# Performance work log

Measured on AMD Instinct MI355X. Metric: run time of the kernel, lower is better.

Reference implementation:

```python
import jax, jax.numpy as jnp
import numpy as np
import math

NUM_EMBED = 1024
EMBED_DIM = 256
COMMITMENT_COST = 0.25


def setup_inputs() -> dict:
    key = jax.random.key(0)
    k1, k2 = jax.random.split(key)
    inputs = jax.random.normal(k1, (16, EMBED_DIM, 4096), dtype=jnp.float32)
    embed = jax.random.normal(k2, (NUM_EMBED, EMBED_DIM), dtype=jnp.float32)
    return {"inputs": inputs, "embed": embed}


def reference(inputs, embed):
    sg = jax.lax.stop_gradient
    num_embed = embed.shape[0]
    # channels-first (B, D, T) -> (B, T, D)
    x = jnp.swapaxes(inputs, 1, -1)
    B, T, D = x.shape
    flat = x.reshape(-1, D)  # (N, D)
    # pairwise squared distances to the codebook: (N, K)
    d2 = (jnp.sum(flat * flat, axis=1, keepdims=True)
          + jnp.sum(embed * embed, axis=1)
          - 2.0 * flat @ embed.T)
    q_idx = jnp.argmin(d2, axis=1)  # (N,) int
    # one-hot @ embed is just a gather of the nearest codewords
    z_q = embed[q_idx].reshape(x.shape)  # (B, T, D)
    vq_loss = jnp.mean((z_q - sg(x)) ** 2)
    commitment_loss = jnp.mean((sg(z_q) - x) ** 2)
    loss = vq_loss + COMMITMENT_COST * commitment_loss
    # straight-through estimator
    z_q_st = x + sg(z_q - x)
    # codebook usage stats: probs = mean of the one-hot rows
    n = flat.shape[0]
    probs = jnp.zeros((num_embed,), dtype=flat.dtype).at[q_idx].add(1.0) / n
    perplexity = jnp.exp(-jnp.sum(probs * jnp.log(probs + 1e-10)))
    num_spatial_positions = n / B  # == T
    kldiv_r = (math.log(num_embed) * num_spatial_positions
               * jnp.ones((B, 1), dtype=x.dtype))
    z_q_out = jnp.swapaxes(z_q_st, 1, -1)  # back to (B, D, T)
    return z_q_out, loss, kldiv_r, perplexity
```

## Files before the change

### kernel.cpp

```cpp
#include <hip/hip_runtime.h>
#include <math.h>

#define T_DIM 4096
#define D_DIM 256
#define K_NUM 1024
#define B_NUM 16
#define N_TOT (B_NUM * T_DIM)
#define EPS_FLAG 0.25f

typedef float f32x4 __attribute__((ext_vector_type(4)));
typedef _Float16 half8 __attribute__((ext_vector_type(8)));

#define WS_FLAGCNT 0
#define WS_LOSS 4
#define WS_DONE 8
#define WS_HIST 64
#define WS_E2 4352
#define WS_QIDX 8704
#define WS_FLAGLIST 270848
#define WS_BESTD 532992
#define WS_ESWZ 795136
#define WS_XROWS 1319424

__device__ inline unsigned umin_(unsigned a, unsigned b) { return a < b ? a : b; }
__device__ inline unsigned umax_(unsigned a, unsigned b) { return a > b ? a : b; }

__global__ __launch_bounds__(256) void prep_kernel(const float* __restrict__ embed,
                                                   unsigned char* __restrict__ eswz,
                                                   float* __restrict__ e2,
                                                   int* __restrict__ wszero) {
    const int tid = threadIdx.x;
    if (blockIdx.x == 0) {
        #pragma unroll
        for (int i = tid; i < 1040; i += 256) wszero[i] = 0;
    }
    const int col = blockIdx.x * 8 + (tid >> 5);
    const int c = tid & 31;
    const float* src = embed + (size_t)col * D_DIM + c * 8;
    half8 h;
    float s = 0.f;
    #pragma unroll
    for (int j = 0; j < 8; ++j) {
        float v = src[j];
        h[j] = (_Float16)v;
        s = fmaf(v, v, s);
    }
    const int g = col >> 4;
    const int k = c >> 2;
    const int l = ((c & 3) << 4) | (col & 15);
    *(half8*)(eswz + (size_t)g * 8192 + k * 1024 + l * 16) = h;
    #pragma unroll
    for (int off = 16; off; off >>= 1) s += __shfl_down(s, off);
    if ((tid & 31) == 0) e2[col] = s;
}

#define LOADB(BUF, P) do {                                                        \
    const unsigned char* _bp = eswz + (size_t)(P) * 8192 + (size_t)(l * 16);      \
    _Pragma("unroll")                                                             \
    for (int _k = 0; _k < 8; ++_k) BUF[_k] = *(const half8*)(_bp + _k * 1024);    \
} while (0)

#define PHASE(BUF, P) do {                                                                     \
    const float _bias = fmaf(e2s[(P) * 16 + (l & 15)], -0.5f, -1024.f);                        \
    f32x4 c0e = {_bias, _bias, _bias, _bias};                                                  \
    f32x4 c1e = {_bias, _bias, _bias, _bias};                                                  \
    f32x4 c0o = {0.f, 0.f, 0.f, 0.f};                                                          \
    f32x4 c1o = {0.f, 0.f, 0.f, 0.f};                                                          \
    c0e = __builtin_amdgcn_mfma_f32_16x16x32_f16(Ah[0][0], BUF[0], c0e, 0, 0, 0);              \
    c1e = __builtin_amdgcn_mfma_f32_16x16x32_f16(Ah[1][0], BUF[0], c1e, 0, 0, 0);              \
    c0o = __builtin_amdgcn_mfma_f32_16x16x32_f16(Ah[0][1], BUF[1], c0o, 0, 0, 0);              \
    c1o = __builtin_amdgcn_mfma_f32_16x16x32_f16(Ah[1][1], BUF[1], c1o, 0, 0, 0);              \
    c0e = __builtin_amdgcn_mfma_f32_16x16x32_f16(Ah[0][2], BUF[2], c0e, 0, 0, 0);              \
    c1e = __builtin_amdgcn_mfma_f32_16x16x32_f16(Ah[1][2], BUF[2], c1e, 0, 0, 0);              \
    c0o = __builtin_amdgcn_mfma_f32_16x16x32_f16(Ah[0][3], BUF[3], c0o, 0, 0, 0);              \
    c1o = __builtin_amdgcn_mfma_f32_16x16x32_f16(Ah[1][3], BUF[3], c1o, 0, 0, 0);              \
    c0e = __builtin_amdgcn_mfma_f32_16x16x32_f16(Ah[0][4], BUF[4], c0e, 0, 0, 0);              \
    c1e = __builtin_amdgcn_mfma_f32_16x16x32_f16(Ah[1][4], BUF[4], c1e, 0, 0, 0);              \
    c0o = __builtin_amdgcn_mfma_f32_16x16x32_f16(Ah[0][5], BUF[5], c0o, 0, 0, 0);              \
    c1o = __builtin_amdgcn_mfma_f32_16x16x32_f16(Ah[1][5], BUF[5], c1o, 0, 0, 0);              \
    c0e = __builtin_amdgcn_mfma_f32_16x16x32_f16(Ah[0][6], BUF[6], c0e, 0, 0, 0);              \
    c1e = __builtin_amdgcn_mfma_f32_16x16x32_f16(Ah[1][6], BUF[6], c1e, 0, 0, 0);              \
    c0o = __builtin_amdgcn_mfma_f32_16x16x32_f16(Ah[0][7], BUF[7], c0o, 0, 0, 0);              \
    c1o = __builtin_amdgcn_mfma_f32_16x16x32_f16(Ah[1][7], BUF[7], c1o, 0, 0, 0);              \
    const unsigned _tag = (unsigned)(P);                                                       \
    _Pragma("unroll")                                                                          \
    for (int _r = 0; _r < 4; ++_r) {                                                           \
        float d0v = (c0e[_r] + c0o[_r]) * -2.f;                                                \
        float d1v = (c1e[_r] + c1o[_r]) * -2.f;                                                \
        unsigned k0 = (__float_as_uint(d0v) & 0xFFFFFFC0u) | _tag;                             \
        unsigned k1 = (__float_as_uint(d1v) & 0xFFFFFFC0u) | _tag;                             \
        unsigned m0 = umax_(bestk[_r], k0);                                                    \
        bestk[_r] = umin_(bestk[_r], k0);                                                      \
        seck[_r] = umin_(seck[_r], m0);                                                        \
        unsigned m1 = umax_(bestk[4 + _r], k1);                                                \
        bestk[4 + _r] = umin_(bestk[4 + _r], k1);                                              \
        seck[4 + _r] = umin_(seck[4 + _r], m1);                                                \
    }                                                                                          \
} while (0)

__global__ __launch_bounds__(256, 2) void argmin_mfma_kernel(
    const float* __restrict__ x, const unsigned char* __restrict__ eswz,
    const float* __restrict__ e2, const float* __restrict__ embed,
    int* __restrict__ qidx, int* __restrict__ flagcnt, int* __restrict__ flaglist,
    float* __restrict__ bestd, float* __restrict__ xrows,
    float* __restrict__ out, int* __restrict__ hist,
    float* __restrict__ loss_sum, int cap)
{
    __shared__ float e2s[K_NUM];
    __shared__ __align__(16) float tile[64 * 128];
    __shared__ int   qid_lds[128];
    __shared__ int   lrows[128];
    __shared__ float lbest[128];
    __shared__ int   lcnt;
    __shared__ int   gbase;

    const int tid = threadIdx.x;
    const int w = tid >> 6;
    const int l = tid & 63;
    const int rb = blockIdx.x * 128;
    const int b = rb >> 12;
    const float* xb = x + (size_t)b * (D_DIM * T_DIM);
    if (tid == 0) lcnt = 0;

    half8 B0[8], B1[8];
    LOADB(B0, 0);

    for (int i = tid; i < K_NUM; i += 256) e2s[i] = e2[i];

    half8 Ah[2][8];
    float x2v[2];
    #pragma unroll
    for (int f = 0; f < 2; ++f) {
        const int row = rb + w * 32 + f * 16 + (l & 15);
        const int t = row & (T_DIM - 1);
        const float* xp = xb + t;
        float s2 = 0.f;
        #pragma unroll
        for (int k = 0; k < 8; ++k) {
            const int d0 = k * 32 + ((l >> 4) << 3);
            half8 h;
            #pragma unroll
            for (int j = 0; j < 8; ++j) {
                float v = xp[(size_t)(d0 + j) * T_DIM];
                h[j] = (_Float16)v;
                s2 = fmaf(v, v, s2);
            }
            Ah[f][k] = h;
        }
        x2v[f] = s2;
    }
    #pragma unroll
    for (int f = 0; f < 2; ++f) {
        x2v[f] += __shfl_xor(x2v[f], 16);
        x2v[f] += __shfl_xor(x2v[f], 32);
    }
    __syncthreads();

    unsigned bestk[8], seck[8];
    #pragma unroll
    for (int s = 0; s < 8; ++s) { bestk[s] = 0xFFFFFFFFu; seck[s] = 0xFFFFFFFFu; }

    for (int pp = 0; pp < 31; ++pp) {
        LOADB(B1, 2 * pp + 1);
        PHASE(B0, 2 * pp);
        LOADB(B0, 2 * pp + 2);
        PHASE(B1, 2 * pp + 1);
    }
    LOADB(B1, 63);
    PHASE(B0, 62);
    PHASE(B1, 63);

    float lossw = 0.f;
    #pragma unroll
    for (int slot = 0; slot < 8; ++slot) {
        float bv = __uint_as_float(bestk[slot] & 0xFFFFFFC0u) - 2048.f;
        float sv = __uint_as_float(seck[slot] & 0xFFFFFFC0u) - 2048.f;
        int bi = (int)(bestk[slot] & 63u) * 16 + (l & 15);
        #pragma unroll
        for (int d = 1; d < 16; d <<= 1) {
            float ob = __shfl_xor(bv, d);
            int   oi = __shfl_xor(bi, d);
            float os = __shfl_xor(sv, d);
            bool take = (ob < bv) || (ob == bv && oi < bi);
            float loser = take ? bv : ob;
            bv = take ? ob : bv;
            bi = take ? oi : bi;
            sv = fminf(fminf(sv, os), loser);
        }
        const int srcl = ((l >> 4) << 2) + (slot & 3);
        const float x2r = __shfl(x2v[slot >> 2], srcl);
        if ((l & 15) == 0) {
            const int rloc = w * 32 + (slot >> 2) * 16 + (l >> 4) * 4 + (slot & 3);
            qidx[rb + rloc] = bi;
            qid_lds[rloc] = bi;
            atomicAdd(&hist[bi], 1);
            lossw += bv + x2r;
            if (sv - bv < EPS_FLAG) {
                int lp = atomicAdd(&lcnt, 1);
                lrows[lp] = rb + rloc;
                lbest[lp] = bv;
            }
        }
    }
    lossw += __shfl_down(lossw, 16);
    lossw += __shfl_down(lossw, 32);
    if (l == 0) atomicAdd(loss_sum, lossw);

    __syncthreads();
    const int nloc = lcnt;
    if (tid == 0) gbase = nloc ? atomicAdd(flagcnt, nloc) : 0;
    __syncthreads();
    for (int i = w; i < nloc; i += 4) {
        const int row = lrows[i];
        const int p = gbase + i;
        const bool have = (p < cap);
        if (have) {
            const float* xp = xb + (row & (T_DIM - 1));
            float4 vv;
            vv.x = xp[(size_t)(l * 4 + 0) * T_DIM];
            vv.y = xp[(size_t)(l * 4 + 1) * T_DIM];
            vv.z = xp[(size_t)(l * 4 + 2) * T_DIM];
            vv.w = xp[(size_t)(l * 4 + 3) * T_DIM];
            *(float4*)(xrows + (size_t)p * D_DIM + l * 4) = vv;
        }
        if (l == 0) {
            flaglist[p] = have ? row : (row | 0x80000000);
            bestd[p] = lbest[i];
        }
    }

    const int t0 = rb & (T_DIM - 1);
    float* outb = out + (size_t)b * (D_DIM * T_DIM);
    for (int c = 0; c < 4; ++c) {
        const int d0 = c * 64;
        __syncthreads();
        {
            const int r = tid & 127;
            const int half = tid >> 7;
            const int qi = qid_lds[r];
            const float4* ep = (const float4*)(embed + (size_t)qi * D_DIM + d0 + half * 32);
            #pragma unroll
            for (int i = 0; i < 8; ++i) {
                const float4 ev = ep[i];
                const int dl = half * 32 + i * 4;
                tile[(dl + 0) * 128 + r] = ev.x;
                tile[(dl + 1) * 128 + r] = ev.y;
                tile[(dl + 2) * 128 + r] = ev.z;
                tile[(dl + 3) * 128 + r] = ev.w;
            }
        }
        __syncthreads();
        #pragma unroll 4
        for (int j = 0; j < 32; ++j) {
            const int flat = j * 256 + tid;
            const int dl = flat >> 7;
            const int rr = flat & 127;
            outb[(size_t)(d0 + dl) * T_DIM + t0 + rr] = tile[dl * 128 + rr];
        }
    }
}

__global__ __launch_bounds__(256) void cleanup_kernel(
    const float* __restrict__ x, const float* __restrict__ xrows,
    const float* __restrict__ embed, const float* __restrict__ e2,
    const int* __restrict__ flagcnt, const int* __restrict__ flaglist,
    int* __restrict__ qidx, const float* __restrict__ bestd,
    float* __restrict__ loss_sum, float* __restrict__ out, int* __restrict__ hist,
    int* __restrict__ donecnt)
{
    __shared__ float xr[8][256];
    __shared__ float rvall[8][256];
    __shared__ int   rixall[8][256];
    __shared__ int   rowss[8];
    __shared__ int   amlast;
    const int tid = threadIdx.x;
    int cnt = flagcnt[0];
    if (cnt > N_TOT) cnt = N_TOT;
    for (int base = blockIdx.x * 8; base < cnt; base += gridDim.x * 8) {
        const int nr = (cnt - base < 8) ? (cnt - base) : 8;
        __syncthreads();
        if (tid < 8) rowss[tid] = (tid < nr) ? flaglist[base + tid] : 0;
        __syncthreads();
        #pragma unroll
        for (int r = 0; r < 8; ++r) {
            float v = 0.f;
            if (r < nr) {
                const int fe = rowss[r];
                if (fe >= 0) {
                    v = xrows[(size_t)(base + r) * D_DIM + tid];
                } else {
                    const int row = fe & 0x7FFFFFFF;
                    v = x[(size_t)(row >> 12) * (D_DIM * T_DIM) + (size_t)tid * T_DIM
                          + (row & (T_DIM - 1))];
                }
            }
            xr[r][tid] = v;
        }
        __syncthreads();

        float bv[8]; int bix[8];
        #pragma unroll
        for (int r = 0; r < 8; ++r) { bv[r] = 3.4e38f; bix[r] = 0x7FFFFFFF; }
        for (int q = 0; q < 4; ++q) {
            const int c = q * 256 + tid;
            const float4* ep = (const float4*)(embed + (size_t)c * D_DIM);
            float acc[8];
            #pragma unroll
            for (int r = 0; r < 8; ++r) acc[r] = 0.f;
            #pragma unroll 8
            for (int dd = 0; dd < 64; ++dd) {
                const float4 ev = ep[dd];
                #pragma unroll
                for (int r = 0; r < 8; ++r) {
                    const float4 xv = *(const float4*)&xr[r][dd * 4];
                    acc[r] = fmaf(ev.x, xv.x, acc[r]);
                    acc[r] = fmaf(ev.y, xv.y, acc[r]);
                    acc[r] = fmaf(ev.z, xv.z, acc[r]);
                    acc[r] = fmaf(ev.w, xv.w, acc[r]);
                }
            }
            const float ec = e2[c];
            #pragma unroll
            for (int r = 0; r < 8; ++r) {
                const float s = fmaf(-2.f, acc[r], ec);
                if (s < bv[r] || (s == bv[r] && c < bix[r])) { bv[r] = s; bix[r] = c; }
            }
        }
        #pragma unroll
        for (int r = 0; r < 8; ++r) { rvall[r][tid] = bv[r]; rixall[r][tid] = bix[r]; }
        __syncthreads();
        const int w = tid >> 6, ll = tid & 63;
        #pragma unroll
        for (int rr2 = 0; rr2 < 2; ++rr2) {
            const int r = w * 2 + rr2;
            float mv = 3.4e38f; int mi = 0x7FFFFFFF;
            #pragma unroll
            for (int j = 0; j < 4; ++j) {
                const float v = rvall[r][ll + j * 64];
                const int i2 = rixall[r][ll + j * 64];
                if (v < mv || (v == mv && i2 < mi)) { mv = v; mi = i2; }
            }
            #pragma unroll
            for (int d = 1; d < 64; d <<= 1) {
                const float ov = __shfl_xor(mv, d);
                const int   oi = __shfl_xor(mi, d);
                if (ov < mv || (ov == mv && oi < mi)) { mv = ov; mi = oi; }
            }
            if (r < nr) {
                const int row = rowss[r] & 0x7FFFFFFF;
                const int old = qidx[row];
                if (mi != old) {
                    const int b2 = row >> 12, t2 = row & (T_DIM - 1);
                    const float4 ev = *(const float4*)(embed + (size_t)mi * D_DIM + ll * 4);
                    float* op = out + (size_t)b2 * (D_DIM * T_DIM) + t2;
                    op[(size_t)(ll * 4 + 0) * T_DIM] = ev.x;
                    op[(size_t)(ll * 4 + 1) * T_DIM] = ev.y;
                    op[(size_t)(ll * 4 + 2) * T_DIM] = ev.z;
                    op[(size_t)(ll * 4 + 3) * T_DIM] = ev.w;
                    if (ll == 0) {
                        qidx[row] = mi;
                        atomicAdd(&hist[mi], 1);
                        atomicAdd(&hist[old], -1);
                    }
                }
                if (ll == 0) atomicAdd(loss_sum, mv - bestd[base + r]);
            }
        }
    }

    __threadfence();
    if (tid == 0) {
        const int old = atomicAdd(donecnt, 1);
        amlast = (old == (int)gridDim.x - 1) ? 1 : 0;
    }
    __syncthreads();
    if (amlast) {
        float acc = 0.f;
        for (int i = tid; i < K_NUM; i += 256) {
            const int h = __hip_atomic_load(&hist[i], __ATOMIC_RELAXED,
                                            __HIP_MEMORY_SCOPE_AGENT);
            const float p = (float)h * (1.f / (float)N_TOT);
            acc += p * logf(p + 1e-10f);
        }
        #pragma unroll
        for (int off = 32; off; off >>= 1) acc += __shfl_down(acc, off);
        __shared__ float ls[4];
        if ((tid & 63) == 0) ls[tid >> 6] = acc;
        __syncthreads();
        if (tid == 0) {
            const float H = -(ls[0] + ls[1] + ls[2] + ls[3]);
            const float L = __hip_atomic_load(loss_sum, __ATOMIC_RELAXED,
                                              __HIP_MEMORY_SCOPE_AGENT);
            const size_t base = (size_t)N_TOT * D_DIM;
            out[base] = 1.25f * L * (1.f / 16777216.f);
            const float kld = (float)(6.931471805599453 * 4096.0);
            #pragma unroll
            for (int i = 0; i < 16; ++i) out[base + 1 + i] = kld;
            out[base + 17] = expf(H);
        }
    }
}

extern "C" void kernel_launch(void* const* d_in, const int* in_sizes, int n_in,
                              void* d_out, int out_size, void* d_ws, size_t ws_size,
                              hipStream_t stream)
{
    const float* x     = (const float*)d_in[0];
    const float* embed = (const float*)d_in[1];
    float* out = (float*)d_out;

    char* ws = (char*)d_ws;
    int*   flagcnt  = (int*)(ws + WS_FLAGCNT);
    float* loss_sum = (float*)(ws + WS_LOSS);
    int*   donecnt  = (int*)(ws + WS_DONE);
    int*   hist     = (int*)(ws + WS_HIST);
    float* e2       = (float*)(ws + WS_E2);
    int*   qidx     = (int*)(ws + WS_QIDX);
    int*   flaglist = (int*)(ws + WS_FLAGLIST);
    float* bestd    = (float*)(ws + WS_BESTD);
    unsigned char* eswz = (unsigned char*)(ws + WS_ESWZ);
    float* xrows    = (float*)(ws + WS_XROWS);

    int cap = 0;
    if (ws_size > (size_t)WS_XROWS + 1024) {
        size_t c = (ws_size - WS_XROWS) / 1024;
        cap = (c > (size_t)N_TOT) ? N_TOT : (int)c;
    }

    prep_kernel<<<128, 256, 0, stream>>>(embed, eswz, e2, (int*)ws);
    argmin_mfma_kernel<<<N_TOT / 128, 256, 0, stream>>>(x, eswz, e2, embed, qidx,
                                                        flagcnt, flaglist, bestd, xrows,
                                                        out, hist, loss_sum, cap);
    cleanup_kernel<<<256, 256, 0, stream>>>(x, xrows, embed, e2, flagcnt, flaglist,
                                            qidx, bestd, loss_sum, out, hist, donecnt);
}
```

Measured before the change: 291.9 us.

## Stage codebook tiles through LDS with async global_load_lds ring buffer

Previously each of the four waves in a block loaded the same swizzled fp16 codebook fragments from global memory straight into registers, double-buffered. Now the block loads each 16 KB codebook chunk once into a four-slot LDS ring using asynchronous global-to-LDS loads, prefetching three chunks ahead. Each chunk is guarded by vmcnt waits and a barrier, and the MFMA phases read their operands from LDS. The aim is to cut redundant global/L2 traffic and register pressure, at the cost of 64 KB of LDS (also reused as the output transpose tile), a barrier per chunk and extra LDS read bandwidth.

```diff
diff --git a/kernel.cpp b/kernel.cpp
--- a/kernel.cpp
+++ b/kernel.cpp
@@ -25,6 +25,12 @@
 __device__ inline unsigned umin_(unsigned a, unsigned b) { return a < b ? a : b; }
 __device__ inline unsigned umax_(unsigned a, unsigned b) { return a > b ? a : b; }
 
+__device__ inline void gl_lds16(const void* g, void* l) {
+    __builtin_amdgcn_global_load_lds(
+        (const __attribute__((address_space(1))) unsigned int*)g,
+        (__attribute__((address_space(3))) unsigned int*)l, 16, 0, 0);
+}
+
 __global__ __launch_bounds__(256) void prep_kernel(const float* __restrict__ embed,
                                                    unsigned char* __restrict__ eswz,
                                                    float* __restrict__ e2,
@@ -54,34 +60,31 @@
     if ((tid & 31) == 0) e2[col] = s;
 }
 
-#define LOADB(BUF, P) do {                                                        \
-    const unsigned char* _bp = eswz + (size_t)(P) * 8192 + (size_t)(l * 16);      \
-    _Pragma("unroll")                                                             \
-    for (int _k = 0; _k < 8; ++_k) BUF[_k] = *(const half8*)(_bp + _k * 1024);    \
-} while (0)
-
-#define PHASE(BUF, P) do {                                                                     \
+#define PHASEL(BBPTR, P) do {                                                                  \
+    half8 Bv[8];                                                                               \
+    _Pragma("unroll")                                                                          \
+    for (int _k = 0; _k < 8; ++_k) Bv[_k] = *(const half8*)((BBPTR) + _k * 1024 + l * 16);     \
     const float _bias = fmaf(e2s[(P) * 16 + (l & 15)], -0.5f, -1024.f);                        \
     f32x4 c0e = {_bias, _bias, _bias, _bias};                                                  \
     f32x4 c1e = {_bias, _bias, _bias, _bias};                                                  \
     f32x4 c0o = {0.f, 0.f, 0.f, 0.f};                                                          \
     f32x4 c1o = {0.f, 0.f, 0.f, 0.f};                                                          \
-    c0e = __builtin_amdgcn_mfma_f32_16x16x32_f16(Ah[0][0], BUF[0], c0e, 0, 0, 0);              \
-    c1e = __builtin_amdgcn_mfma_f32_16x16x32_f16(Ah[1][0], BUF[0], c1e, 0, 0, 0);              \
-    c0o = __builtin_amdgcn_mfma_f32_16x16x32_f16(Ah[0][1], BUF[1], c0o, 0, 0, 0);              \
-    c1o = __builtin_amdgcn_mfma_f32_16x16x32_f16(Ah[1][1], BUF[1], c1o, 0, 0, 0);              \
-    c0e = __builtin_amdgcn_mfma_f32_16x16x32_f16(Ah[0][2], BUF[2], c0e, 0, 0, 0);              \
-    c1e = __builtin_amdgcn_mfma_f32_16x16x32_f16(Ah[1][2], BUF[2], c1e, 0, 0, 0);              \
-    c0o = __builtin_amdgcn_mfma_f32_16x16x32_f16(Ah[0][3], BUF[3], c0o, 0, 0, 0);              \
-    c1o = __builtin_amdgcn_mfma_f32_16x16x32_f16(Ah[1][3], BUF[3], c1o, 0, 0, 0);              \
-    c0e = __builtin_amdgcn_mfma_f32_16x16x32_f16(Ah[0][4], BUF[4], c0e, 0, 0, 0);              \
-    c1e = __builtin_amdgcn_mfma_f32_16x16x32_f16(Ah[1][4], BUF[4], c1e, 0, 0, 0);              \
-    c0o = __builtin_amdgcn_mfma_f32_16x16x32_f16(Ah[0][5], BUF[5], c0o, 0, 0, 0);              \
-    c1o = __builtin_amdgcn_mfma_f32_16x16x32_f16(Ah[1][5], BUF[5], c1o, 0, 0, 0);              \
-    c0e = __builtin_amdgcn_mfma_f32_16x16x32_f16(Ah[0][6], BUF[6], c0e, 0, 0, 0);              \
-    c1e = __builtin_amdgcn_mfma_f32_16x16x32_f16(Ah[1][6], BUF[6], c1e, 0, 0, 0);              \
-    c0o = __builtin_amdgcn_mfma_f32_16x16x32_f16(Ah[0][7], BUF[7], c0o, 0, 0, 0);              \
-    c1o = __builtin_amdgcn_mfma_f32_16x16x32_f16(Ah[1][7], BUF[7], c1o, 0, 0, 0);              \
+    c0e = __builtin_amdgcn_mfma_f32_16x16x32_f16(Ah[0][0], Bv[0], c0e, 0, 0, 0);               \
+    c1e = __builtin_amdgcn_mfma_f32_16x16x32_f16(Ah[1][0], Bv[0], c1e, 0, 0, 0);               \
+    c0o = __builtin_amdgcn_mfma_f32_16x16x32_f16(Ah[0][1], Bv[1], c0o, 0, 0, 0);               \
+    c1o = __builtin_amdgcn_mfma_f32_16x16x32_f16(Ah[1][1], Bv[1], c1o, 0, 0, 0);               \
+    c0e = __builtin_amdgcn_mfma_f32_16x16x32_f16(Ah[0][2], Bv[2], c0e, 0, 0, 0);               \
+    c1e = __builtin_amdgcn_mfma_f32_16x16x32_f16(Ah[1][2], Bv[2], c1e, 0, 0, 0);               \
+    c0o = __builtin_amdgcn_mfma_f32_16x16x32_f16(Ah[0][3], Bv[3], c0o, 0, 0, 0);               \
+    c1o = __builtin_amdgcn_mfma_f32_16x16x32_f16(Ah[1][3], Bv[3], c1o, 0, 0, 0);               \
+    c0e = __builtin_amdgcn_mfma_f32_16x16x32_f16(Ah[0][4], Bv[4], c0e, 0, 0, 0);               \
+    c1e = __builtin_amdgcn_mfma_f32_16x16x32_f16(Ah[1][4], Bv[4], c1e, 0, 0, 0);               \
+    c0o = __builtin_amdgcn_mfma_f32_16x16x32_f16(Ah[0][5], Bv[5], c0o, 0, 0, 0);               \
+    c1o = __builtin_amdgcn_mfma_f32_16x16x32_f16(Ah[1][5], Bv[5], c1o, 0, 0, 0);               \
+    c0e = __builtin_amdgcn_mfma_f32_16x16x32_f16(Ah[0][6], Bv[6], c0e, 0, 0, 0);               \
+    c1e = __builtin_amdgcn_mfma_f32_16x16x32_f16(Ah[1][6], Bv[6], c1e, 0, 0, 0);               \
+    c0o = __builtin_amdgcn_mfma_f32_16x16x32_f16(Ah[0][7], Bv[7], c0o, 0, 0, 0);               \
+    c1o = __builtin_amdgcn_mfma_f32_16x16x32_f16(Ah[1][7], Bv[7], c1o, 0, 0, 0);               \
     const unsigned _tag = (unsigned)(P);                                                       \
     _Pragma("unroll")                                                                          \
     for (int _r = 0; _r < 4; ++_r) {                                                           \
@@ -106,8 +109,8 @@
     float* __restrict__ out, int* __restrict__ hist,
     float* __restrict__ loss_sum, int cap)
 {
+    __shared__ __align__(16) unsigned char bbuf[4][16384];
     __shared__ float e2s[K_NUM];
-    __shared__ __align__(16) float tile[64 * 128];
     __shared__ int   qid_lds[128];
     __shared__ int   lrows[128];
     __shared__ float lbest[128];
@@ -122,9 +125,13 @@
     const float* xb = x + (size_t)b * (D_DIM * T_DIM);
     if (tid == 0) lcnt = 0;
 
-    half8 B0[8], B1[8];
-    LOADB(B0, 0);
-
+    #pragma unroll
+    for (int c0 = 0; c0 < 3; ++c0) {
+        const unsigned char* src = eswz + (size_t)c0 * 16384 + (size_t)tid * 16;
+        unsigned char* dst = &bbuf[c0][tid * 16];
+        #pragma unroll
+        for (int r = 0; r < 4; ++r) gl_lds16(src + r * 4096, dst + r * 4096);
+    }
     for (int i = tid; i < K_NUM; i += 256) e2s[i] = e2[i];
 
     half8 Ah[2][8];
@@ -160,15 +167,21 @@
     #pragma unroll
     for (int s = 0; s < 8; ++s) { bestk[s] = 0xFFFFFFFFu; seck[s] = 0xFFFFFFFFu; }
 
-    for (int pp = 0; pp < 31; ++pp) {
-        LOADB(B1, 2 * pp + 1);
-        PHASE(B0, 2 * pp);
-        LOADB(B0, 2 * pp + 2);
-        PHASE(B1, 2 * pp + 1);
-    }
-    LOADB(B1, 63);
-    PHASE(B0, 62);
-    PHASE(B1, 63);
+    for (int c = 0; c < 32; ++c) {
+        if (c <= 29)      asm volatile("s_waitcnt vmcnt(8)" ::: "memory");
+        else if (c == 30) asm volatile("s_waitcnt vmcnt(4)" ::: "memory");
+        else              asm volatile("s_waitcnt vmcnt(0)" ::: "memory");
+        __builtin_amdgcn_s_barrier();
+        if (c + 3 < 32) {
+            const unsigned char* src = eswz + (size_t)(c + 3) * 16384 + (size_t)tid * 16;
+            unsigned char* dst = &bbuf[(c + 3) & 3][tid * 16];
+            #pragma unroll
+            for (int r = 0; r < 4; ++r) gl_lds16(src + r * 4096, dst + r * 4096);
+        }
+        const unsigned char* bbc = bbuf[c & 3];
+        PHASEL(bbc, 2 * c);
+        PHASEL(bbc + 8192, 2 * c + 1);
+    }
 
     float lossw = 0.f;
     #pragma unroll
@@ -229,6 +242,7 @@
         }
     }
 
+    float* tile = (float*)bbuf;
     const int t0 = rb & (T_DIM - 1);
     float* outb = out + (size_t)b * (D_DIM * T_DIM);
     for (int c = 0; c < 4; ++c) {
```

After: 296.7 us. About the same (+1.6%).
